# Kernel tuning notes

Hardware: AMD Instinct MI355X
Metric: run time of the kernel (lower is better)

Reference implementation:

```python
import jax, jax.numpy as jnp
import numpy as np

N, A, C, S = 65536, 1024, 1000, 2  # S = max aug multiplier from self.augs


def _update_cv(x, labels, cov_prior, ave_prior, amount_prior):
    # Efficient segment-reduce form of update_CV (original builds O(N*C*A) onehot tensor)
    cnt = jax.ops.segment_sum(jnp.ones((N,), x.dtype), labels, num_segments=C)  # [C]
    sum_c = jax.ops.segment_sum(x, labels, num_segments=C)                      # [C,A]
    cnt_c = jnp.where(cnt == 0, 1.0, cnt)                                       # Amount_CxA clamp
    ave = sum_c / cnt_c[:, None]                                                # ave_CxA
    var = jax.ops.segment_sum((x - ave[labels]) ** 2, labels, num_segments=C) / cnt_c[:, None]
    var = jnp.where(var == 0, 1e-10, var)
    w = (cnt / (cnt + amount_prior + 1e-10))[:, None]                           # weight_CV [C,1]
    additional = w * (1 - w) * (ave_prior - ave) ** 2
    new_cov = cov_prior * (1 - w) + var * w + additional
    new_ave = ave_prior * (1 - w) + ave * w
    new_amount = amount_prior + cnt
    return new_cov, new_ave, new_amount


def setup_inputs() -> dict:
    key = jax.random.key(0)
    ks = jax.random.split(key, 6)
    return {
        "x": jax.random.normal(ks[0], (N, A), jnp.float32),
        "eps": jax.random.normal(ks[1], (S, C, A), jnp.float32),
        "fc_w": jax.random.normal(ks[2], (C, A), jnp.float32) * 0.02,
        "fc_b": jnp.zeros((C,), jnp.float32),
        "ba_coeffi": jax.random.normal(ks[3], (C,), jnp.float32) * 0.1,
        "cov_prior": jax.random.uniform(ks[4], (C, A), jnp.float32) * 0.01,
        "ave_prior": jnp.zeros((C, A), jnp.float32),
        "amount_prior": jnp.zeros((C,), jnp.float32),
        "target_x": jax.random.randint(ks[5], (N,), 0, C).astype(jnp.int64),
    }


def reference(x, eps, fc_w, fc_b, ba_coeffi, cov_prior, ave_prior, amount_prior, target_x):
    # update_CV runs under torch.no_grad -> stop_gradient on stats
    new_cov, new_ave, _ = _update_cv(x, target_x, cov_prior, ave_prior, amount_prior)
    new_cov = jax.lax.stop_gradient(new_cov)
    new_ave = jax.lax.stop_gradient(new_ave)
    # Gaussian augmentation: Normal(loc=Ave, scale=CoVariance).sample((S,)) per class
    aug = new_ave[None, :, :] + new_cov[None, :, :] * eps  # [S,C,A]
    aug = aug.reshape(S * C, A)
    aug_labels = jnp.tile(jnp.arange(C, dtype=target_x.dtype), S)
    feats = jnp.concatenate([x, aug], axis=0)              # [N+S*C, A]
    labels_all = jnp.concatenate([target_x, aug_labels], axis=0)
    logits = feats @ fc_w.T + fc_b - ba_coeffi             # [N+S*C, C]
    logp = jax.nn.log_softmax(logits, axis=-1)
    loss = -jnp.mean(jnp.take_along_axis(logp, labels_all[:, None], axis=1))
    return loss
```

## Files before the change

kernel.cpp:

```cpp
#include <hip/hip_runtime.h>

#define NROWS 65536
#define ADIM  1024
#define CCLS  1000
#define SAUG  2
#define MROWS (NROWS + SAUG*CCLS)
#define MPAD  67584
#define NPAD  1024
#define NSPLIT 4
#define NEG_INF (-3.0e38f)

typedef __bf16 bf16x8 __attribute__((ext_vector_type(8)));
typedef float  f32x4  __attribute__((ext_vector_type(4)));
typedef unsigned short u16;

__device__ __forceinline__ unsigned pk2bf(float a, float b){
  unsigned ua = __float_as_uint(a), ub = __float_as_uint(b);
  ua = (ua + 0x7FFFu + ((ua>>16)&1u)) >> 16;
  ub = (ub + 0x7FFFu + ((ub>>16)&1u)) >> 16;
  return ua | (ub<<16);
}

__global__ void k_hist(const int* __restrict__ tgt, int* __restrict__ cnt){
  int i = blockIdx.x*blockDim.x + threadIdx.x;
  int stride = gridDim.x*blockDim.x;
  for (; i < NROWS; i += stride) atomicAdd(&cnt[tgt[i]], 1);
}

__global__ void k_scan(const int* __restrict__ cnt, int* __restrict__ start){
  __shared__ int s[1024];
  int t = threadIdx.x;
  int v = (t < CCLS) ? cnt[t] : 0;
  s[t] = v;
  __syncthreads();
  for (int off = 1; off < 1024; off <<= 1){
    int u = (t >= off) ? s[t-off] : 0;
    __syncthreads();
    s[t] += u;
    __syncthreads();
  }
  if (t < CCLS) start[t] = s[t] - v;
}

__global__ void k_scatter(const int* __restrict__ tgt, const int* __restrict__ start,
                          int* __restrict__ pos, int* __restrict__ sorted){
  int i = blockIdx.x*blockDim.x + threadIdx.x;
  int stride = gridDim.x*blockDim.x;
  for (; i < NROWS; i += stride){
    int c = tgt[i];
    int r = atomicAdd(&pos[c], 1);
    sorted[start[c] + r] = i;
  }
}

__global__ void k_cvt_x(const float* __restrict__ x, u16* __restrict__ xb){
  size_t i = ((size_t)blockIdx.x*blockDim.x + threadIdx.x)*8;
  float4 a = *(const float4*)(x+i);
  float4 b = *(const float4*)(x+i+4);
  uint4 o;
  o.x = pk2bf(a.x,a.y); o.y = pk2bf(a.z,a.w);
  o.z = pk2bf(b.x,b.y); o.w = pk2bf(b.z,b.w);
  *(uint4*)(xb+i) = o;
}

__global__ void k_pad(u16* __restrict__ xb){
  size_t i = ((size_t)blockIdx.x*blockDim.x + threadIdx.x)*8 + (size_t)MROWS*ADIM;
  uint4 z = {0u,0u,0u,0u};
  *(uint4*)(xb+i) = z;
}

__global__ void k_cvt_w(const float* __restrict__ w, u16* __restrict__ wb){
  size_t i = ((size_t)blockIdx.x*blockDim.x + threadIdx.x)*8;
  int row = (int)(i >> 10);
  uint4 o = {0u,0u,0u,0u};
  if (row < CCLS){
    float4 a = *(const float4*)(w+i);
    float4 b = *(const float4*)(w+i+4);
    o.x = pk2bf(a.x,a.y); o.y = pk2bf(a.z,a.w);
    o.z = pk2bf(b.x,b.y); o.w = pk2bf(b.z,b.w);
  }
  *(uint4*)(wb+i) = o;
}

__global__ void k_bias(const float* __restrict__ fc_b, const float* __restrict__ ba,
                       float* __restrict__ biasv){
  int c = blockIdx.x*blockDim.x + threadIdx.x;
  if (c < NPAD) biasv[c] = (c < CCLS) ? fc_b[c] - ba[c] : NEG_INF;
}

__global__ void k_stats(const float* __restrict__ x, const int* __restrict__ sorted,
                        const int* __restrict__ cnt, const int* __restrict__ start,
                        const float* __restrict__ amt_p, const float* __restrict__ cov_p,
                        const float* __restrict__ ave_p, const float* __restrict__ eps,
                        u16* __restrict__ xb){
  int c = blockIdx.x;
  int t = threadIdx.x;
  int col = t*4;
  int n = cnt[c];
  int st = start[c];
  float s[4] = {0.f,0.f,0.f,0.f}, q[4] = {0.f,0.f,0.f,0.f};
  for (int i = 0; i < n; i++){
    int row = sorted[st + i];
    const float4 v = *(const float4*)(x + (size_t)row*ADIM + col);
    s[0]+=v.x; s[1]+=v.y; s[2]+=v.z; s[3]+=v.w;
    q[0]+=v.x*v.x; q[1]+=v.y*v.y; q[2]+=v.z*v.z; q[3]+=v.w*v.w;
  }
  float cf = (float)n;
  float cc = (n == 0) ? 1.f : cf;
  float wgt = cf / (cf + amt_p[c] + 1e-10f);
  float4 cv = *(const float4*)(cov_p + (size_t)c*ADIM + col);
  float4 av = *(const float4*)(ave_p + (size_t)c*ADIM + col);
  float cvp[4] = {cv.x,cv.y,cv.z,cv.w};
  float avp[4] = {av.x,av.y,av.z,av.w};
  float ncov[4], nave[4];
  #pragma unroll
  for (int j = 0; j < 4; j++){
    float ave = s[j]/cc;
    float var = (q[j] - 2.f*ave*s[j] + cf*ave*ave)/cc;
    if (var <= 0.f) var = 1e-10f;
    float add = wgt*(1.f-wgt)*(avp[j]-ave)*(avp[j]-ave);
    ncov[j] = cvp[j]*(1.f-wgt) + var*wgt + add;
    nave[j] = avp[j]*(1.f-wgt) + ave*wgt;
  }
  #pragma unroll
  for (int s_ = 0; s_ < SAUG; s_++){
    size_t eoff = ((size_t)(s_*CCLS + c))*ADIM + col;
    size_t roff = ((size_t)(NROWS + s_*CCLS + c))*ADIM + col;
    const float4 e = *(const float4*)(eps + eoff);
    uint2 o;
    o.x = pk2bf(nave[0]+ncov[0]*e.x, nave[1]+ncov[1]*e.y);
    o.y = pk2bf(nave[2]+ncov[2]*e.z, nave[3]+ncov[3]*e.w);
    *(uint2*)(xb + roff) = o;
  }
}

__global__ __launch_bounds__(256,2) void k_gemm_part(
    const u16* __restrict__ xb, const u16* __restrict__ wb,
    const float* __restrict__ biasv, const int* __restrict__ tgt,
    float* __restrict__ pm, float* __restrict__ pl, float* __restrict__ plab){
  __shared__ char smem[16384] __attribute__((aligned(16)));
  char* smA = smem;
  char* smB = smem + 8192;
  const int t = threadIdx.x;
  const int lane = t & 63;
  const int wv = t >> 6;
  const int quad = lane >> 4;
  const int col = lane & 15;
  const int row0 = blockIdx.x * 128;
  const int sp = blockIdx.y;

  int lbl[8];
  #pragma unroll
  for (int i = 0; i < 8; i++){
    int gr = row0 + wv*32 + (i>>2)*16 + quad*4 + (i&3);
    int l = -1;
    if (gr < NROWS) l = tgt[gr];
    else if (gr < MROWS){ int a = gr - NROWS; l = (a < CCLS) ? a : a - CCLS; }
    lbl[i] = l;
  }
  float m_run[8], l_run[8], lab[8];
  #pragma unroll
  for (int i = 0; i < 8; i++){ m_run[i] = NEG_INF; l_run[i] = 0.f; lab[i] = NEG_INF; }

  const u16* ga0 = xb + (size_t)row0*ADIM;

  for (int ci = 0; ci < 2; ci++){
    const int nb = sp*2 + ci;
    const u16* gb0 = wb + (size_t)(nb*128)*ADIM;
    f32x4 acc[2][8];
    const f32x4 z = {0.f,0.f,0.f,0.f};
    #pragma unroll
    for (int sm = 0; sm < 2; sm++)
      #pragma unroll
      for (int sn = 0; sn < 8; sn++) acc[sm][sn] = z;

    for (int kc = 0; kc < ADIM/32; kc++){
      __syncthreads();
      #pragma unroll
      for (int i = 0; i < 2; i++){
        int o = i*4096 + t*16;
        int row = o >> 6;
        int kp  = (o >> 4) & 3;
        const u16* g = ga0 + (size_t)row*ADIM + kc*32 + kp*8;
        __builtin_amdgcn_global_load_lds((const __attribute__((address_space(1))) void*)g,
            (__attribute__((address_space(3))) void*)(smA + i*4096 + wv*1024), 16, 0, 0);
        const u16* g2 = gb0 + (size_t)row*ADIM + kc*32 + kp*8;
        __builtin_amdgcn_global_load_lds((const __attribute__((address_space(1))) void*)g2,
            (__attribute__((address_space(3))) void*)(smB + i*4096 + wv*1024), 16, 0, 0);
      }
      __syncthreads();
      bf16x8 af[2], bfr[8];
      const int kq = quad*16;
      #pragma unroll
      for (int sm = 0; sm < 2; sm++){
        int r = wv*32 + sm*16 + col;
        af[sm] = *(const bf16x8*)(smA + r*64 + kq);
      }
      #pragma unroll
      for (int sn = 0; sn < 8; sn++){
        int n = sn*16 + col;
        bfr[sn] = *(const bf16x8*)(smB + n*64 + kq);
      }
      #pragma unroll
      for (int sm = 0; sm < 2; sm++)
        #pragma unroll
        for (int sn = 0; sn < 8; sn++)
          acc[sm][sn] = __builtin_amdgcn_mfma_f32_16x16x32_bf16(af[sm], bfr[sn], acc[sm][sn], 0, 0, 0);
    }

    float bias[8];
    #pragma unroll
    for (int sn = 0; sn < 8; sn++) bias[sn] = biasv[nb*128 + sn*16 + col];
    #pragma unroll
    for (int i = 0; i < 8; i++){
      const int sm = i>>2, rg = i&3;
      float lg[8];
      float mx = NEG_INF, lv = NEG_INF;
      #pragma unroll
      for (int sn = 0; sn < 8; sn++){
        float v = acc[sm][sn][rg] + bias[sn];
        lg[sn] = v;
        mx = fmaxf(mx, v);
        int c = nb*128 + sn*16 + col;
        lv = (c == lbl[i]) ? v : lv;
      }
      #pragma unroll
      for (int o = 1; o < 16; o <<= 1) mx = fmaxf(mx, __shfl_xor(mx, o));
      float mnew = fmaxf(m_run[i], mx);
      float se = 0.f;
      #pragma unroll
      for (int sn = 0; sn < 8; sn++) se += __expf(lg[sn] - mnew);
      #pragma unroll
      for (int o = 1; o < 16; o <<= 1) se += __shfl_xor(se, o);
      l_run[i] = l_run[i]*__expf(m_run[i] - mnew) + se;
      m_run[i] = mnew;
      #pragma unroll
      for (int o = 1; o < 16; o <<= 1) lv = fmaxf(lv, __shfl_xor(lv, o));
      lab[i] = fmaxf(lab[i], lv);
    }
  }

  if (col == 0){
    #pragma unroll
    for (int i = 0; i < 8; i++){
      int gr = row0 + wv*32 + (i>>2)*16 + quad*4 + (i&3);
      size_t idx = (size_t)sp*MPAD + gr;
      pm[idx]   = m_run[i];
      pl[idx]   = l_run[i];
      plab[idx] = lab[i];
    }
  }
}

__global__ void k_merge(const float* __restrict__ pm, const float* __restrict__ pl,
                        const float* __restrict__ plab, float* __restrict__ loss){
  int r = blockIdx.x*256 + threadIdx.x;
  float v = 0.f;
  if (r < MROWS){
    float m = NEG_INF, lb = NEG_INF;
    #pragma unroll
    for (int s = 0; s < NSPLIT; s++){
      m  = fmaxf(m,  pm[(size_t)s*MPAD + r]);
      lb = fmaxf(lb, plab[(size_t)s*MPAD + r]);
    }
    float l = 0.f;
    #pragma unroll
    for (int s = 0; s < NSPLIT; s++)
      l += pl[(size_t)s*MPAD + r]*__expf(pm[(size_t)s*MPAD + r] - m);
    v = m + __logf(l) - lb;
  }
  #pragma unroll
  for (int o = 32; o > 0; o >>= 1) v += __shfl_xor(v, o);
  if ((threadIdx.x & 63) == 0) atomicAdd(loss, v);
}

__global__ void k_final(const float* __restrict__ loss, float* __restrict__ out){
  out[0] = loss[0] * (1.0f/(float)MROWS);
}

extern "C" void kernel_launch(void* const* d_in, const int* in_sizes, int n_in,
                              void* d_out, int out_size, void* d_ws, size_t ws_size,
                              hipStream_t stream) {
  const float* x     = (const float*)d_in[0];
  const float* eps   = (const float*)d_in[1];
  const float* fc_w  = (const float*)d_in[2];
  const float* fc_b  = (const float*)d_in[3];
  const float* ba    = (const float*)d_in[4];
  const float* cov_p = (const float*)d_in[5];
  const float* ave_p = (const float*)d_in[6];
  const float* amt_p = (const float*)d_in[7];
  const int*   tgt   = (const int*)d_in[8];
  float* out = (float*)d_out;

  char* ws = (char*)d_ws;
  u16*   xb    = (u16*)(ws);
  u16*   wb    = (u16*)(ws + 138412032u);
  float* biasv = (float*)(ws + 140509184u);
  int*   sorted= (int*)(ws + 140513280u);
  int*   cnt   = (int*)(ws + 140775424u);
  int*   pos   = (int*)(ws + 140779520u);
  int*   start = (int*)(ws + 140783616u);
  float* loss  = (float*)(ws + 140787712u);
  float* pm    = (float*)(ws + 140791808u);
  float* pl    = (float*)(ws + 141873152u);
  float* plab  = (float*)(ws + 142954496u);

  hipMemsetAsync(cnt, 0, 16384, stream);

  k_hist   <<<256, 256, 0, stream>>>(tgt, cnt);
  k_scan   <<<1, 1024, 0, stream>>>(cnt, start);
  k_scatter<<<256, 256, 0, stream>>>(tgt, start, pos, sorted);
  k_cvt_x  <<<32768, 256, 0, stream>>>(x, xb);
  k_pad    <<<24, 256, 0, stream>>>(xb);
  k_cvt_w  <<<512, 256, 0, stream>>>(fc_w, wb);
  k_bias   <<<4, 256, 0, stream>>>(fc_b, ba, biasv);
  k_stats  <<<CCLS, 256, 0, stream>>>(x, sorted, cnt, start, amt_p, cov_p, ave_p, eps, xb);
  k_gemm_part<<<dim3(528, 4), 256, 0, stream>>>(xb, wb, biasv, tgt, pm, pl, plab);
  k_merge  <<<264, 256, 0, stream>>>(pm, pl, plab, loss);
  k_final  <<<1, 1, 0, stream>>>(loss, out);
}
```

Before: 774.0 us.

## Widen GEMM tile to 128x256, read bf16 x in stats, fuse final scale

Result: faster. 701.1 us (-9.4%).

```diff
diff --git a/kernel.cpp b/kernel.cpp
--- a/kernel.cpp
+++ b/kernel.cpp
@@ -7,7 +7,7 @@
 #define MROWS (NROWS + SAUG*CCLS)
 #define MPAD  67584
 #define NPAD  1024
-#define NSPLIT 4
+#define NPART 8
 #define NEG_INF (-3.0e38f)
 
 typedef __bf16 bf16x8 __attribute__((ext_vector_type(8)));
@@ -20,6 +20,8 @@
   ub = (ub + 0x7FFFu + ((ub>>16)&1u)) >> 16;
   return ua | (ub<<16);
 }
+__device__ __forceinline__ float bflo(unsigned u){ return __uint_as_float((u & 0xFFFFu) << 16); }
+__device__ __forceinline__ float bfhi(unsigned u){ return __uint_as_float(u & 0xFFFF0000u); }
 
 __global__ void k_hist(const int* __restrict__ tgt, int* __restrict__ cnt){
   int i = blockIdx.x*blockDim.x + threadIdx.x;
@@ -88,7 +90,7 @@
   if (c < NPAD) biasv[c] = (c < CCLS) ? fc_b[c] - ba[c] : NEG_INF;
 }
 
-__global__ void k_stats(const float* __restrict__ x, const int* __restrict__ sorted,
+__global__ void k_stats(const u16* __restrict__ xb_in, const int* __restrict__ sorted,
                         const int* __restrict__ cnt, const int* __restrict__ start,
                         const float* __restrict__ amt_p, const float* __restrict__ cov_p,
                         const float* __restrict__ ave_p, const float* __restrict__ eps,
@@ -101,9 +103,10 @@
   float s[4] = {0.f,0.f,0.f,0.f}, q[4] = {0.f,0.f,0.f,0.f};
   for (int i = 0; i < n; i++){
     int row = sorted[st + i];
-    const float4 v = *(const float4*)(x + (size_t)row*ADIM + col);
-    s[0]+=v.x; s[1]+=v.y; s[2]+=v.z; s[3]+=v.w;
-    q[0]+=v.x*v.x; q[1]+=v.y*v.y; q[2]+=v.z*v.z; q[3]+=v.w*v.w;
+    const uint2 uv = *(const uint2*)(xb_in + (size_t)row*ADIM + col);
+    float v0 = bflo(uv.x), v1 = bfhi(uv.x), v2 = bflo(uv.y), v3 = bfhi(uv.y);
+    s[0]+=v0; s[1]+=v1; s[2]+=v2; s[3]+=v3;
+    q[0]+=v0*v0; q[1]+=v1*v1; q[2]+=v2*v2; q[3]+=v3*v3;
   }
   float cf = (float)n;
   float cc = (n == 0) ? 1.f : cf;
@@ -138,144 +141,123 @@
     const u16* __restrict__ xb, const u16* __restrict__ wb,
     const float* __restrict__ biasv, const int* __restrict__ tgt,
     float* __restrict__ pm, float* __restrict__ pl, float* __restrict__ plab){
-  __shared__ char smem[16384] __attribute__((aligned(16)));
+  __shared__ char smem[24576] __attribute__((aligned(16)));
   char* smA = smem;
   char* smB = smem + 8192;
   const int t = threadIdx.x;
   const int lane = t & 63;
   const int wv = t >> 6;
+  const int rh = wv & 1;
+  const int ch = wv >> 1;
   const int quad = lane >> 4;
   const int col = lane & 15;
-  const int row0 = blockIdx.x * 128;
-  const int sp = blockIdx.y;
-
-  int lbl[8];
-  #pragma unroll
-  for (int i = 0; i < 8; i++){
-    int gr = row0 + wv*32 + (i>>2)*16 + quad*4 + (i&3);
-    int l = -1;
-    if (gr < NROWS) l = tgt[gr];
-    else if (gr < MROWS){ int a = gr - NROWS; l = (a < CCLS) ? a : a - CCLS; }
-    lbl[i] = l;
-  }
-  float m_run[8], l_run[8], lab[8];
-  #pragma unroll
-  for (int i = 0; i < 8; i++){ m_run[i] = NEG_INF; l_run[i] = 0.f; lab[i] = NEG_INF; }
-
-  const u16* ga0 = xb + (size_t)row0*ADIM;
-
-  for (int ci = 0; ci < 2; ci++){
-    const int nb = sp*2 + ci;
-    const u16* gb0 = wb + (size_t)(nb*128)*ADIM;
-    f32x4 acc[2][8];
-    const f32x4 z = {0.f,0.f,0.f,0.f};
-    #pragma unroll
-    for (int sm = 0; sm < 2; sm++)
+  const int row0 = blockIdx.y * 128;
+  const int sp = blockIdx.x;
+
+  f32x4 acc[4][8];
+  const f32x4 z = {0.f,0.f,0.f,0.f};
+  #pragma unroll
+  for (int sm = 0; sm < 4; sm++)
+    #pragma unroll
+    for (int sn = 0; sn < 8; sn++) acc[sm][sn] = z;
+
+  const u16* ga = xb + (size_t)row0*ADIM;
+  const u16* gb = wb + (size_t)(sp*256)*ADIM;
+
+  for (int kc = 0; kc < ADIM/32; kc++){
+    __syncthreads();
+    #pragma unroll
+    for (int i = 0; i < 2; i++){
+      int o = wv*2048 + i*1024 + lane*16;
+      const u16* g = ga + (size_t)(o>>6)*ADIM + kc*32 + ((o>>4)&3)*8;
+      __builtin_amdgcn_global_load_lds((const __attribute__((address_space(1))) void*)g,
+          (__attribute__((address_space(3))) void*)(smA + wv*2048 + i*1024), 16, 0, 0);
+    }
+    #pragma unroll
+    for (int i = 0; i < 4; i++){
+      int o = wv*4096 + i*1024 + lane*16;
+      const u16* g = gb + (size_t)(o>>6)*ADIM + kc*32 + ((o>>4)&3)*8;
+      __builtin_amdgcn_global_load_lds((const __attribute__((address_space(1))) void*)g,
+          (__attribute__((address_space(3))) void*)(smB + wv*4096 + i*1024), 16, 0, 0);
+    }
+    __syncthreads();
+    bf16x8 af[4], bfr[8];
+    const int kq = quad*16;
+    #pragma unroll
+    for (int sm = 0; sm < 4; sm++){
+      int r = rh*64 + sm*16 + col;
+      af[sm] = *(const bf16x8*)(smA + r*64 + kq);
+    }
+    #pragma unroll
+    for (int sn = 0; sn < 8; sn++){
+      int n = ch*128 + sn*16 + col;
+      bfr[sn] = *(const bf16x8*)(smB + n*64 + kq);
+    }
+    #pragma unroll
+    for (int sm = 0; sm < 4; sm++)
       #pragma unroll
-      for (int sn = 0; sn < 8; sn++) acc[sm][sn] = z;
-
-    for (int kc = 0; kc < ADIM/32; kc++){
-      __syncthreads();
-      #pragma unroll
-      for (int i = 0; i < 2; i++){
-        int o = i*4096 + t*16;
-        int row = o >> 6;
-        int kp  = (o >> 4) & 3;
-        const u16* g = ga0 + (size_t)row*ADIM + kc*32 + kp*8;
-        __builtin_amdgcn_global_load_lds((const __attribute__((address_space(1))) void*)g,
-            (__attribute__((address_space(3))) void*)(smA + i*4096 + wv*1024), 16, 0, 0);
-        const u16* g2 = gb0 + (size_t)row*ADIM + kc*32 + kp*8;
-        __builtin_amdgcn_global_load_lds((const __attribute__((address_space(1))) void*)g2,
-            (__attribute__((address_space(3))) void*)(smB + i*4096 + wv*1024), 16, 0, 0);
-      }
-      __syncthreads();
-      bf16x8 af[2], bfr[8];
-      const int kq = quad*16;
-      #pragma unroll
-      for (int sm = 0; sm < 2; sm++){
-        int r = wv*32 + sm*16 + col;
-        af[sm] = *(const bf16x8*)(smA + r*64 + kq);
-      }
-      #pragma unroll
-      for (int sn = 0; sn < 8; sn++){
-        int n = sn*16 + col;
-        bfr[sn] = *(const bf16x8*)(smB + n*64 + kq);
-      }
-      #pragma unroll
-      for (int sm = 0; sm < 2; sm++)
-        #pragma unroll
-        for (int sn = 0; sn < 8; sn++)
-          acc[sm][sn] = __builtin_amdgcn_mfma_f32_16x16x32_bf16(af[sm], bfr[sn], acc[sm][sn], 0, 0, 0);
-    }
-
-    float bias[8];
-    #pragma unroll
-    for (int sn = 0; sn < 8; sn++) bias[sn] = biasv[nb*128 + sn*16 + col];
-    #pragma unroll
-    for (int i = 0; i < 8; i++){
-      const int sm = i>>2, rg = i&3;
-      float lg[8];
-      float mx = NEG_INF, lv = NEG_INF;
-      #pragma unroll
-      for (int sn = 0; sn < 8; sn++){
-        float v = acc[sm][sn][rg] + bias[sn];
-        lg[sn] = v;
-        mx = fmaxf(mx, v);
-        int c = nb*128 + sn*16 + col;
-        lv = (c == lbl[i]) ? v : lv;
-      }
-      #pragma unroll
-      for (int o = 1; o < 16; o <<= 1) mx = fmaxf(mx, __shfl_xor(mx, o));
-      float mnew = fmaxf(m_run[i], mx);
-      float se = 0.f;
-      #pragma unroll
-      for (int sn = 0; sn < 8; sn++) se += __expf(lg[sn] - mnew);
-      #pragma unroll
-      for (int o = 1; o < 16; o <<= 1) se += __shfl_xor(se, o);
-      l_run[i] = l_run[i]*__expf(m_run[i] - mnew) + se;
-      m_run[i] = mnew;
-      #pragma unroll
-      for (int o = 1; o < 16; o <<= 1) lv = fmaxf(lv, __shfl_xor(lv, o));
-      lab[i] = fmaxf(lab[i], lv);
-    }
-  }
-
-  if (col == 0){
-    #pragma unroll
-    for (int i = 0; i < 8; i++){
-      int gr = row0 + wv*32 + (i>>2)*16 + quad*4 + (i&3);
-      size_t idx = (size_t)sp*MPAD + gr;
-      pm[idx]   = m_run[i];
-      pl[idx]   = l_run[i];
-      plab[idx] = lab[i];
+      for (int sn = 0; sn < 8; sn++)
+        acc[sm][sn] = __builtin_amdgcn_mfma_f32_16x16x32_bf16(af[sm], bfr[sn], acc[sm][sn], 0, 0, 0);
+  }
+
+  float bias[8];
+  #pragma unroll
+  for (int sn = 0; sn < 8; sn++) bias[sn] = biasv[sp*256 + ch*128 + sn*16 + col];
+  #pragma unroll
+  for (int i = 0; i < 16; i++){
+    const int sm = i>>2, rg = i&3;
+    const int gr = row0 + rh*64 + sm*16 + quad*4 + rg;
+    int lbl = -1;
+    if (gr < NROWS) lbl = tgt[gr];
+    else if (gr < MROWS){ int a = gr - NROWS; lbl = (a < CCLS) ? a : a - CCLS; }
+    float lg[8];
+    float mx = NEG_INF, lv = NEG_INF;
+    #pragma unroll
+    for (int sn = 0; sn < 8; sn++){
+      float v = acc[sm][sn][rg] + bias[sn];
+      lg[sn] = v;
+      mx = fmaxf(mx, v);
+      int c = sp*256 + ch*128 + sn*16 + col;
+      lv = (c == lbl) ? v : lv;
+    }
+    #pragma unroll
+    for (int o = 1; o < 16; o <<= 1) mx = fmaxf(mx, __shfl_xor(mx, o));
+    float se = 0.f;
+    #pragma unroll
+    for (int sn = 0; sn < 8; sn++) se += __expf(lg[sn] - mx);
+    #pragma unroll
+    for (int o = 1; o < 16; o <<= 1) se += __shfl_xor(se, o);
+    #pragma unroll
+    for (int o = 1; o < 16; o <<= 1) lv = fmaxf(lv, __shfl_xor(lv, o));
+    if (col == 0){
+      size_t idx = (size_t)(sp*2 + ch)*MPAD + gr;
+      pm[idx]   = mx;
+      pl[idx]   = se;
+      plab[idx] = lv;
     }
   }
 }
 
 __global__ void k_merge(const float* __restrict__ pm, const float* __restrict__ pl,
-                        const float* __restrict__ plab, float* __restrict__ loss){
+                        const float* __restrict__ plab, float* __restrict__ out){
   int r = blockIdx.x*256 + threadIdx.x;
   float v = 0.f;
   if (r < MROWS){
     float m = NEG_INF, lb = NEG_INF;
     #pragma unroll
-    for (int s = 0; s < NSPLIT; s++){
+    for (int s = 0; s < NPART; s++){
       m  = fmaxf(m,  pm[(size_t)s*MPAD + r]);
       lb = fmaxf(lb, plab[(size_t)s*MPAD + r]);
     }
     float l = 0.f;
     #pragma unroll
-    for (int s = 0; s < NSPLIT; s++)
+    for (int s = 0; s < NPART; s++)
       l += pl[(size_t)s*MPAD + r]*__expf(pm[(size_t)s*MPAD + r] - m);
-    v = m + __logf(l) - lb;
+    v = (m + __logf(l) - lb) * (1.0f/(float)MROWS);
   }
   #pragma unroll
   for (int o = 32; o > 0; o >>= 1) v += __shfl_xor(v, o);
-  if ((threadIdx.x & 63) == 0) atomicAdd(loss, v);
-}
-
-__global__ void k_final(const float* __restrict__ loss, float* __restrict__ out){
-  out[0] = loss[0] * (1.0f/(float)MROWS);
+  if ((threadIdx.x & 63) == 0) atomicAdd(out, v);
 }
 
 extern "C" void kernel_launch(void* const* d_in, const int* in_sizes, int n_in,
@@ -300,12 +282,12 @@
   int*   cnt   = (int*)(ws + 140775424u);
   int*   pos   = (int*)(ws + 140779520u);
   int*   start = (int*)(ws + 140783616u);
-  float* loss  = (float*)(ws + 140787712u);
-  float* pm    = (float*)(ws + 140791808u);
-  float* pl    = (float*)(ws + 141873152u);
-  float* plab  = (float*)(ws + 142954496u);
-
-  hipMemsetAsync(cnt, 0, 16384, stream);
+  float* pm    = (float*)(ws + 140787712u);
+  float* pl    = (float*)(ws + 142950400u);
+  float* plab  = (float*)(ws + 145113088u);
+
+  hipMemsetAsync(cnt, 0, 12288, stream);
+  hipMemsetAsync(out, 0, sizeof(float), stream);
 
   k_hist   <<<256, 256, 0, stream>>>(tgt, cnt);
   k_scan   <<<1, 1024, 0, stream>>>(cnt, start);
@@ -314,8 +296,7 @@
   k_pad    <<<24, 256, 0, stream>>>(xb);
   k_cvt_w  <<<512, 256, 0, stream>>>(fc_w, wb);
   k_bias   <<<4, 256, 0, stream>>>(fc_b, ba, biasv);
-  k_stats  <<<CCLS, 256, 0, stream>>>(x, sorted, cnt, start, amt_p, cov_p, ave_p, eps, xb);
-  k_gemm_part<<<dim3(528, 4), 256, 0, stream>>>(xb, wb, biasv, tgt, pm, pl, plab);
-  k_merge  <<<264, 256, 0, stream>>>(pm, pl, plab, loss);
-  k_final  <<<1, 1, 0, stream>>>(loss, out);
-}
+  k_stats  <<<CCLS, 256, 0, stream>>>(xb, sorted, cnt, start, amt_p, cov_p, ave_p, eps, xb);
+  k_gemm_part<<<dim3(4, 528), 256, 0, stream>>>(xb, wb, biasv, tgt, pm, pl, plab);
+  k_merge  <<<264, 256, 0, stream>>>(pm, pl, plab, out);
+}
```
